# Kernel optimization log

Hardware: AMD Instinct MI355X
Metric: run time of the kernel (lower is better)

The kernel has to match this reference:

```python
import jax, jax.numpy as jnp
import numpy as np

N_NODES = 50000
N_EDGES = 500000
N_REL = 8
D = 128        # input_dim
A_DIM = 64     # attention_dim
D_OUT = 128    # output_dim


def setup_inputs() -> dict:
    key = jax.random.key(0)
    ks = jax.random.split(key, 10)
    h = jax.random.normal(ks[0], (N_NODES, D), jnp.float32)
    # relation gate tables: [R, 2*D, D]; first D rows act on dst (subject), last D on src (object)
    relations = jax.random.normal(ks[1], (N_REL, 2 * D, D), jnp.float32) * 0.05
    rel_attention = jax.random.normal(ks[2], (N_REL, A_DIM), jnp.float32) * 0.05
    W_a = jax.random.normal(ks[3], (A_DIM, 2 * D), jnp.float32) * 0.05
    b_a = jnp.zeros((A_DIM,), jnp.float32)
    W_lin = jax.random.normal(ks[4], (D_OUT, 2 * D), jnp.float32) * 0.05
    b_lin = jnp.zeros((D_OUT,), jnp.float32)
    src = jax.random.randint(ks[5], (N_EDGES,), 0, N_NODES, dtype=jnp.int32)
    dst = jax.random.randint(ks[6], (N_EDGES,), 0, N_NODES, dtype=jnp.int32)
    etype = jax.random.randint(ks[7], (N_EDGES,), 0, N_REL, dtype=jnp.int32)
    return {"h": h, "relations": relations, "rel_attention": rel_attention,
            "W_a": W_a, "b_a": b_a, "W_lin": W_lin, "b_lin": b_lin,
            "src": src, "dst": dst, "etype": etype}


def reference(h, relations, rel_attention, W_a, b_a, W_lin, b_lin, src, dst, etype):
    d = h.shape[-1]
    # --- gates: relation-indexed gather_mm (concat gate type) ---
    # Project every node through every relation once (R is small), then gather per edge.
    proj_dst = jnp.einsum('nd,rde->rne', h, relations[:, :d, :])   # [R, N, D] subject/dst side
    proj_src = jnp.einsum('nd,rde->rne', h, relations[:, d:, :])   # [R, N, D] object/src side
    gate = jax.nn.sigmoid(proj_dst[etype, dst] + proj_src[etype, src])  # [E, D]

    src_h = h[src]   # [E, D]
    dst_h = h[dst]   # [E, D]

    # --- gatv2 attention (predicates are zeroed in the module -> rel_attention[0]) ---
    a = jax.nn.leaky_relu(jnp.concatenate([dst_h, src_h], axis=-1) @ W_a.T + b_a)  # [E, A]
    score = (rel_attention[0] * a).sum(-1)  # [E]

    # --- edge_softmax over destination-node segments ---
    smax = jax.ops.segment_max(score, dst, num_segments=N_NODES)
    ex = jnp.exp(score - smax[dst])
    denom = jax.ops.segment_sum(ex, dst, num_segments=N_NODES)
    attn = ex / denom[dst]  # [E]

    # --- message = u_mul_e(h, attn*gate), reduce = sum over dst ---
    msg = src_h * (attn[:, None] * gate)                 # [E, D]
    h_N = jax.ops.segment_sum(msg, dst, num_segments=N_NODES)  # [N, D]

    # --- graphsage aggregate: LeakyReLU(W [h ; h_N] + b) ---
    out = jax.nn.leaky_relu(jnp.concatenate([h, h_N], axis=-1) @ W_lin.T + b_lin)
    return out
```

## Files before the change

kernel.cpp:

```cpp
#include <hip/hip_runtime.h>
#include <cstdint>
#include <cstddef>

constexpr int NNODES = 50000;
constexpr int NEDGES = 500000;
constexpr int NRELS  = 8;
constexpr int DIM    = 128;
constexpr int ADIM   = 64;
constexpr int TWOD   = 256;
constexpr int EPB    = 64;
constexpr float SLOPE = 0.01f;

constexpr int XPITCH = TWOD + 8;
constexpr int PPITCH = DIM + 8;
constexpr int MPITCH = DIM + 8;
constexpr int SPAD = NEDGES + 1024;

typedef __attribute__((ext_vector_type(8))) short short8;
typedef __attribute__((ext_vector_type(4))) float floatx4;

__device__ __forceinline__ unsigned short f2bf(float f) {
    unsigned u = __float_as_uint(f);
    unsigned r = u + 0x7FFFu + ((u >> 16) & 1u);
    return (unsigned short)(r >> 16);
}
__device__ __forceinline__ float bf2f(unsigned short b) {
    return __uint_as_float(((unsigned)b) << 16);
}

__global__ void k_init(int* __restrict__ srcS, int* __restrict__ histD,
                       int* __restrict__ cursorD, int* __restrict__ cnts) {
    int i = blockIdx.x * blockDim.x + threadIdx.x;
    int stride = gridDim.x * blockDim.x;
    for (int idx = i; idx < SPAD; idx += stride) srcS[idx] = -1;
    for (int idx = i; idx < NNODES; idx += stride) { histD[idx] = 0; cursorD[idx] = 0; }
    if (i < 16) cnts[i] = 0;
}

__global__ __launch_bounds__(256) void k_prep(const float* __restrict__ rel,
                                              const float* __restrict__ W_lin,
                                              const float* __restrict__ W_a,
                                              unsigned short* __restrict__ relT,
                                              unsigned short* __restrict__ Wl,
                                              unsigned short* __restrict__ Wa2) {
    __shared__ float ls[64][65];
    int b = blockIdx.x, t = threadIdx.x;
    if (b < 64) {
        int r = b >> 3, tile = b & 7;
        int d0 = (tile >> 1) * 64, o0 = (tile & 1) * 64;
        const float* rp = rel + ((size_t)r * TWOD + d0) * DIM + o0;
#pragma unroll
        for (int u = 0; u < 16; u++) {
            int v = u * 256 + t;
            int j = v & 63, i = v >> 6;
            ls[i][j] = rp[(size_t)i * DIM + j];
        }
        __syncthreads();
        unsigned short* wp = relT + ((size_t)r * DIM + o0) * TWOD + d0;
#pragma unroll
        for (int u = 0; u < 16; u++) {
            int v = u * 256 + t;
            int ii = v & 63, jj = v >> 6;
            wp[(size_t)jj * TWOD + ii] = f2bf(ls[ii][jj]);
        }
    } else {
        int idx = (b - 64) * 256 + t;
        if (idx < DIM * TWOD) {
            Wl[idx] = f2bf(W_lin[idx]);
        } else {
            int j = idx - DIM * TWOD;
            if (j < DIM * DIM) {
                int d = j & 127, o = j >> 7;
                float v = (o < ADIM) ? W_a[(size_t)o * TWOD + d]
                                     : W_a[(size_t)(o - ADIM) * TWOD + DIM + d];
                Wa2[j] = f2bf(v);
            }
        }
    }
}

__global__ void k_hist2(const int* __restrict__ ety, const int* __restrict__ dst,
                        int* __restrict__ cnt, int* __restrict__ histD) {
    __shared__ int hist[NRELS];
    int t = threadIdx.x;
    if (t < NRELS) hist[t] = 0;
    __syncthreads();
    int e = blockIdx.x * 256 + t;
    if (e < NEDGES) {
        atomicAdd(&hist[ety[e]], 1);
        atomicAdd(&histD[dst[e]], 1);
    }
    __syncthreads();
    if (t < NRELS && hist[t] > 0) atomicAdd(&cnt[t], hist[t]);
}

__global__ __launch_bounds__(1024) void k_scan(const int* __restrict__ histD,
                                               int* __restrict__ row_ptr,
                                               const int* __restrict__ cnt,
                                               int* __restrict__ offs) {
    __shared__ int ls[1024];
    const int t = threadIdx.x;
    const int CH = (NNODES + 1023) / 1024;
    const int base = t * CH;
    int s = 0;
    for (int j = 0; j < CH; j++) { int i = base + j; if (i < NNODES) s += histD[i]; }
    ls[t] = s;
    __syncthreads();
    for (int off = 1; off < 1024; off <<= 1) {
        int v = (t >= off) ? ls[t - off] : 0;
        __syncthreads();
        ls[t] += v;
        __syncthreads();
    }
    int run = (t == 0) ? 0 : ls[t - 1];
    for (int j = 0; j < CH; j++) {
        int i = base + j;
        if (i < NNODES) { row_ptr[i] = run; run += histD[i]; }
    }
    if (t == 1023) row_ptr[NNODES] = ls[1023];
    if (t == 0) {
        int off = 0;
        for (int r = 0; r < NRELS; r++) {
            offs[r] = off;
            off += ((cnt[r] + EPB - 1) / EPB) * EPB;
        }
    }
}

__global__ void k_dscatter(const int* __restrict__ ety, const int* __restrict__ src,
                           const int* __restrict__ dst, const int* __restrict__ row_ptr,
                           int* __restrict__ cursorD,
                           int* __restrict__ srcP, int* __restrict__ dstP,
                           int* __restrict__ etyP) {
    int e = blockIdx.x * 256 + threadIdx.x;
    if (e < NEDGES) {
        int dn = dst[e];
        int pos = row_ptr[dn] + atomicAdd(&cursorD[dn], 1);
        srcP[pos] = src[e];
        dstP[pos] = dn;
        etyP[pos] = ety[e];
    }
}

__global__ void k_scatter3(const int* __restrict__ srcP, const int* __restrict__ dstP,
                           const int* __restrict__ etyP, const int* __restrict__ offs,
                           int* __restrict__ cursorE,
                           int* __restrict__ srcS, int* __restrict__ dstS,
                           int* __restrict__ posS) {
    __shared__ int hist[NRELS];
    __shared__ int basew[NRELS];
    int t = threadIdx.x;
    if (t < NRELS) hist[t] = 0;
    __syncthreads();
    int p = blockIdx.x * 256 + t;
    int r = -1, rank = 0, sn = 0, dn = 0;
    if (p < NEDGES) {
        r = etyP[p]; sn = srcP[p]; dn = dstP[p];
        rank = atomicAdd(&hist[r], 1);
    }
    __syncthreads();
    if (t < NRELS && hist[t] > 0) basew[t] = atomicAdd(&cursorE[t], hist[t]);
    __syncthreads();
    if (p < NEDGES) {
        int s = offs[r] + basew[r] + rank;
        srcS[s] = sn;
        dstS[s] = dn;
        posS[s] = p;
    }
}

__global__ __launch_bounds__(256) void k_nodeproj(const float* __restrict__ h,
                                                  const unsigned short* __restrict__ Wa2,
                                                  unsigned short* __restrict__ proj16,
                                                  unsigned short* __restrict__ h16) {
    __shared__ unsigned short Xs[EPB * PPITCH];
    const int t = threadIdx.x;
    const int nb = blockIdx.x * 64;

#pragma unroll
    for (int u = 0; u < 4; u++) {
        int v = u * 256 + t;
        int i = v >> 4;
        int c = v & 15;
        int n = nb + i;
        bool ok = n < NNODES;
        if (!ok) n = NNODES - 1;
        const float4* hp = (const float4*)(h + (size_t)n * DIM + c * 8);
        float4 a = hp[0], b = hp[1];
        union { unsigned short us[8]; short8 s8; } pk;
        pk.us[0] = f2bf(a.x); pk.us[1] = f2bf(a.y); pk.us[2] = f2bf(a.z); pk.us[3] = f2bf(a.w);
        pk.us[4] = f2bf(b.x); pk.us[5] = f2bf(b.y); pk.us[6] = f2bf(b.z); pk.us[7] = f2bf(b.w);
        *(short8*)&Xs[i * PPITCH + c * 8] = pk.s8;
        if (ok) *(short8*)&h16[(size_t)n * DIM + c * 8] = pk.s8;
    }

    const int wave = t >> 6;
    const int lane = t & 63;
    const int q = lane >> 4;
    const int l16 = lane & 15;

    short8 Bf[2][4];
#pragma unroll
    for (int nn = 0; nn < 2; nn++) {
        int o = (wave * 2 + nn) * 16 + l16;
        const unsigned short* bp = Wa2 + (size_t)o * DIM + q * 8;
#pragma unroll
        for (int ks = 0; ks < 4; ks++) Bf[nn][ks] = *(const short8*)(bp + ks * 32);
    }

    __syncthreads();

    floatx4 acc[4][2];
#pragma unroll
    for (int m = 0; m < 4; m++)
#pragma unroll
        for (int nn = 0; nn < 2; nn++) acc[m][nn] = (floatx4)(0.0f);

#pragma unroll
    for (int ks = 0; ks < 4; ks++) {
        short8 Af[4];
        const unsigned short* xb = &Xs[l16 * PPITCH + ks * 32 + q * 8];
#pragma unroll
        for (int m = 0; m < 4; m++) Af[m] = *(const short8*)(xb + m * 16 * PPITCH);
#pragma unroll
        for (int m = 0; m < 4; m++)
#pragma unroll
            for (int nn = 0; nn < 2; nn++)
                acc[m][nn] = __builtin_amdgcn_mfma_f32_16x16x32_bf16(Af[m], Bf[nn][ks], acc[m][nn], 0, 0, 0);
    }

#pragma unroll
    for (int m = 0; m < 4; m++) {
        int ib = m * 16 + q * 4;
#pragma unroll
        for (int nn = 0; nn < 2; nn++) {
            int o = (wave * 2 + nn) * 16 + l16;
#pragma unroll
            for (int rg = 0; rg < 4; rg++) {
                int n = nb + ib + rg;
                if (n < NNODES) proj16[(size_t)n * DIM + o] = f2bf(acc[m][nn][rg]);
            }
        }
    }
}

__global__ __launch_bounds__(256) void k_score(const unsigned short* __restrict__ proj16,
                                               const float* __restrict__ b_a, const float* __restrict__ ratt,
                                               const int* __restrict__ srcP, const int* __restrict__ dstP,
                                               float* __restrict__ scoreP) {
    int p = blockIdx.x * 4 + (threadIdx.x >> 6);
    int lane = threadIdx.x & 63;
    if (p >= NEDGES) return;
    int sn = srcP[p], dn = dstP[p];
    float v = bf2f(proj16[(size_t)dn * DIM + lane]) + bf2f(proj16[(size_t)sn * DIM + ADIM + lane]) + b_a[lane];
    v = v > 0.0f ? v : SLOPE * v;
    v *= ratt[lane];
#pragma unroll
    for (int off = 32; off > 0; off >>= 1) v += __shfl_down(v, off);
    if (lane == 0) scoreP[p] = v;
}

__global__ __launch_bounds__(256) void k_segsoft(float* __restrict__ scoreP,
                                                 const int* __restrict__ row_ptr) {
    int n = blockIdx.x * 16 + (threadIdx.x >> 4);
    int l = threadIdx.x & 15;
    if (n >= NNODES) return;
    int p0 = row_ptr[n], p1 = row_ptr[n + 1];
    if (p0 >= p1) return;
    float m = -3.0e38f;
    for (int p = p0 + l; p < p1; p += 16) m = fmaxf(m, scoreP[p]);
#pragma unroll
    for (int off = 8; off > 0; off >>= 1) m = fmaxf(m, __shfl_xor(m, off, 16));
    float sum = 0.0f;
    for (int p = p0 + l; p < p1; p += 16) {
        float x = __expf(scoreP[p] - m);
        scoreP[p] = x;
        sum += x;
    }
#pragma unroll
    for (int off = 8; off > 0; off >>= 1) sum += __shfl_xor(sum, off, 16);
    float inv = 1.0f / sum;
    for (int p = p0 + l; p < p1; p += 16) scoreP[p] *= inv;
}

__global__ __launch_bounds__(256) void k_gate_msg(
    const unsigned short* __restrict__ h16, const unsigned short* __restrict__ relT,
    const int* __restrict__ srcS, const int* __restrict__ dstS, const int* __restrict__ posS,
    const int* __restrict__ offs,
    unsigned short* __restrict__ msgbuf) {
    __shared__ unsigned short Xs[EPB * XPITCH];
    __shared__ unsigned short Ms[EPB * MPITCH];
    __shared__ int srcn_s[EPB];
    __shared__ int dstn_s[EPB];
    __shared__ int pos_s[EPB];
    __shared__ int val_s[EPB];

    const int t = threadIdx.x;
    const int base = blockIdx.x * EPB;

    if (t < EPB) {
        int s = base + t;
        int sv = srcS[s];
        int valid = sv >= 0;
        val_s[t] = valid;
        srcn_s[t] = valid ? sv : 0;
        dstn_s[t] = valid ? dstS[s] : 0;
        pos_s[t] = valid ? posS[s] : 0;
    }
    __syncthreads();
    if (!val_s[0]) return;

    int r = 0;
#pragma unroll
    for (int i = 1; i < NRELS; i++) if (base >= offs[i]) r = i;

#pragma unroll
    for (int u = 0; u < 8; u++) {
        int v = u * 256 + t;
        int i = v >> 5;
        int c = v & 31;
        int node = (c < 16) ? dstn_s[i] : srcn_s[i];
        *(short8*)&Xs[i * XPITCH + c * 8] = *(const short8*)&h16[(size_t)node * DIM + (c & 15) * 8];
    }

    const int wave = t >> 6;
    const int lane = t & 63;
    const int q = lane >> 4;
    const int l16 = lane & 15;

    short8 Bf[2][8];
#pragma unroll
    for (int nn = 0; nn < 2; nn++) {
        int o = (wave * 2 + nn) * 16 + l16;
        const unsigned short* bp = relT + ((size_t)r * DIM + o) * TWOD + q * 8;
#pragma unroll
        for (int ks = 0; ks < 8; ks++) Bf[nn][ks] = *(const short8*)(bp + ks * 32);
    }

    __syncthreads();

    floatx4 acc[4][2];
#pragma unroll
    for (int m = 0; m < 4; m++)
#pragma unroll
        for (int nn = 0; nn < 2; nn++) acc[m][nn] = (floatx4)(0.0f);

#pragma unroll
    for (int ks = 0; ks < 8; ks++) {
        short8 Af[4];
        const unsigned short* xb = &Xs[l16 * XPITCH + ks * 32 + q * 8];
#pragma unroll
        for (int m = 0; m < 4; m++) Af[m] = *(const short8*)(xb + m * 16 * XPITCH);
#pragma unroll
        for (int m = 0; m < 4; m++)
#pragma unroll
            for (int nn = 0; nn < 2; nn++)
                acc[m][nn] = __builtin_amdgcn_mfma_f32_16x16x32_bf16(Af[m], Bf[nn][ks], acc[m][nn], 0, 0, 0);
    }

#pragma unroll
    for (int m = 0; m < 4; m++) {
        int ib = m * 16 + q * 4;
#pragma unroll
        for (int nn = 0; nn < 2; nn++) {
            int o = (wave * 2 + nn) * 16 + l16;
#pragma unroll
            for (int rg = 0; rg < 4; rg++) {
                int i = ib + rg;
                float g = 1.0f / (1.0f + __expf(-acc[m][nn][rg]));
                float sh = bf2f(Xs[i * XPITCH + DIM + o]);
                Ms[i * MPITCH + o] = f2bf(sh * g);
            }
        }
    }
    __syncthreads();
#pragma unroll
    for (int u = 0; u < 4; u++) {
        int v = u * 256 + t;
        int i = v >> 4;
        int c = v & 15;
        if (!val_s[i]) continue;
        short8 val = *(const short8*)&Ms[i * MPITCH + c * 8];
        *(short8*)&msgbuf[(size_t)pos_s[i] * DIM + c * 8] = val;
    }
}

__global__ __launch_bounds__(256) void k_aggr(const unsigned short* __restrict__ msgbuf,
                                              const float* __restrict__ attP,
                                              const int* __restrict__ row_ptr,
                                              unsigned short* __restrict__ hN16) {
    int n = blockIdx.x * 4 + (threadIdx.x >> 6);
    int lane = threadIdx.x & 63;
    if (n >= NNODES) return;
    int p0 = row_ptr[n], p1 = row_ptr[n + 1];
    float a0 = 0.0f, a1 = 0.0f;
    for (int p = p0; p < p1; p++) {
        float at = attP[p];
        unsigned v = *(const unsigned*)&msgbuf[(size_t)p * DIM + lane * 2];
        a0 += at * bf2f((unsigned short)(v & 0xFFFFu));
        a1 += at * bf2f((unsigned short)(v >> 16));
    }
    unsigned o = (unsigned)f2bf(a0) | ((unsigned)f2bf(a1) << 16);
    *(unsigned*)&hN16[(size_t)n * DIM + lane * 2] = o;
}

__global__ __launch_bounds__(256) void k_out(const unsigned short* __restrict__ h16,
                                             const unsigned short* __restrict__ hN16,
                                             const unsigned short* __restrict__ Wl,
                                             const float* __restrict__ b_lin,
                                             float* __restrict__ out) {
    __shared__ unsigned short Xs[EPB * XPITCH];
    const int t = threadIdx.x;
    const int nb = blockIdx.x * 64;

#pragma unroll
    for (int u = 0; u < 8; u++) {
        int v = u * 256 + t;
        int i = v >> 5;
        int c = v & 31;
        int n = nb + i;
        if (n >= NNODES) n = NNODES - 1;
        const unsigned short* srcp = (c < 16) ? h16 : hN16;
        *(short8*)&Xs[i * XPITCH + c * 8] = *(const short8*)&srcp[(size_t)n * DIM + (c & 15) * 8];
    }

    const int wave = t >> 6;
    const int lane = t & 63;
    const int q = lane >> 4;
    const int l16 = lane & 15;

    short8 Bf[2][8];
#pragma unroll
    for (int nn = 0; nn < 2; nn++) {
        int o = (wave * 2 + nn) * 16 + l16;
        const unsigned short* bp = Wl + (size_t)o * TWOD + q * 8;
#pragma unroll
        for (int ks = 0; ks < 8; ks++) Bf[nn][ks] = *(const short8*)(bp + ks * 32);
    }

    __syncthreads();

    floatx4 acc[4][2];
#pragma unroll
    for (int m = 0; m < 4; m++)
#pragma unroll
        for (int nn = 0; nn < 2; nn++) acc[m][nn] = (floatx4)(0.0f);

#pragma unroll
    for (int ks = 0; ks < 8; ks++) {
        short8 Af[4];
        const unsigned short* xb = &Xs[l16 * XPITCH + ks * 32 + q * 8];
#pragma unroll
        for (int m = 0; m < 4; m++) Af[m] = *(const short8*)(xb + m * 16 * XPITCH);
#pragma unroll
        for (int m = 0; m < 4; m++)
#pragma unroll
            for (int nn = 0; nn < 2; nn++)
                acc[m][nn] = __builtin_amdgcn_mfma_f32_16x16x32_bf16(Af[m], Bf[nn][ks], acc[m][nn], 0, 0, 0);
    }

#pragma unroll
    for (int m = 0; m < 4; m++) {
        int ib = m * 16 + q * 4;
#pragma unroll
        for (int nn = 0; nn < 2; nn++) {
            int o = (wave * 2 + nn) * 16 + l16;
            float bl = b_lin[o];
#pragma unroll
            for (int rg = 0; rg < 4; rg++) {
                int n = nb + ib + rg;
                if (n < NNODES) {
                    float val = acc[m][nn][rg] + bl;
                    val = val > 0.0f ? val : SLOPE * val;
                    out[(size_t)n * DIM + o] = val;
                }
            }
        }
    }
}

extern "C" void kernel_launch(void* const* d_in, const int* in_sizes, int n_in,
                              void* d_out, int out_size, void* d_ws, size_t ws_size,
                              hipStream_t stream) {
    const float* h     = (const float*)d_in[0];
    const float* rel   = (const float*)d_in[1];
    const float* ratt  = (const float*)d_in[2];
    const float* W_a   = (const float*)d_in[3];
    const float* b_a   = (const float*)d_in[4];
    const float* W_lin = (const float*)d_in[5];
    const float* b_lin = (const float*)d_in[6];
    const int* src = (const int*)d_in[7];
    const int* dst = (const int*)d_in[8];
    const int* ety = (const int*)d_in[9];
    float* out = (float*)d_out;

    float* scoreP = (float*)d_ws;
    unsigned short* h16    = (unsigned short*)(scoreP + NEDGES);
    unsigned short* proj16 = h16 + (size_t)NNODES * DIM;
    unsigned short* hN16   = proj16 + (size_t)NNODES * DIM;
    unsigned short* relT   = hN16 + (size_t)NNODES * DIM;
    unsigned short* Wl     = relT + (size_t)NRELS * DIM * TWOD;
    unsigned short* Wa2    = Wl + (size_t)DIM * TWOD;
    int* srcS    = (int*)(Wa2 + (size_t)DIM * DIM);
    int* dstS    = srcS + SPAD;
    int* posS    = dstS + SPAD;
    int* srcP    = posS + SPAD;
    int* dstP    = srcP + NEDGES;
    int* etyP    = dstP + NEDGES;
    int* row_ptr = etyP + NEDGES;
    int* histD   = row_ptr + (NNODES + 1);
    int* cursorD = histD + NNODES;
    int* cnts    = cursorD + NNODES;
    int* offs    = cnts + 16;
    unsigned short* msgbuf = (unsigned short*)(((uintptr_t)(offs + 8) + 255) & ~(uintptr_t)255);

    k_init<<<2048, 256, 0, stream>>>(srcS, histD, cursorD, cnts);
    k_prep<<<64 + (DIM * TWOD + DIM * DIM + 255) / 256, 256, 0, stream>>>(
        rel, W_lin, W_a, relT, Wl, Wa2);
    k_hist2<<<(NEDGES + 255) / 256, 256, 0, stream>>>(ety, dst, cnts, histD);
    k_scan<<<1, 1024, 0, stream>>>(histD, row_ptr, cnts, offs);
    k_dscatter<<<(NEDGES + 255) / 256, 256, 0, stream>>>(
        ety, src, dst, row_ptr, cursorD, srcP, dstP, etyP);
    k_nodeproj<<<(NNODES + 63) / 64, 256, 0, stream>>>(h, Wa2, proj16, h16);
    k_scatter3<<<(NEDGES + 255) / 256, 256, 0, stream>>>(
        srcP, dstP, etyP, offs, cnts + 8, srcS, dstS, posS);
    k_score<<<(NEDGES + 3) / 4, 256, 0, stream>>>(proj16, b_a, ratt, srcP, dstP, scoreP);
    k_segsoft<<<(NNODES + 15) / 16, 256, 0, stream>>>(scoreP, row_ptr);
    k_gate_msg<<<(NEDGES + 8 * EPB + EPB - 1) / EPB, 256, 0, stream>>>(
        h16, relT, srcS, dstS, posS, offs, msgbuf);
    k_aggr<<<(NNODES + 3) / 4, 256, 0, stream>>>(msgbuf, scoreP, row_ptr, hN16);
    k_out<<<(NNODES + 63) / 64, 256, 0, stream>>>(h16, hN16, Wl, b_lin, out);
}
```

Before: 553.8 us.

## Fuse attention score into gate-message kernel and pack edge metadata into int4

Attention scores are now computed per edge inside the gate/message kernel. An extra MFMA pass multiplies the already-gathered [dst;src] bf16 tile by W_a, which replaces the per-node projection kernel and the separate score kernel. Edge metadata (src, dst, type, position) is packed into int4 records so each scatter stage does one vector access instead of several scalar arrays, and the message is written back into the staging tile in place of a second shared buffer. In exchange, the attention GEMM is redone per edge rather than per node (about ten times more FLOPs), and the gate kernel carries extra register and shared-memory pressure.

```diff
diff --git a/kernel.cpp b/kernel.cpp
--- a/kernel.cpp
+++ b/kernel.cpp
@@ -12,8 +12,6 @@
 constexpr float SLOPE = 0.01f;
 
 constexpr int XPITCH = TWOD + 8;
-constexpr int PPITCH = DIM + 8;
-constexpr int MPITCH = DIM + 8;
 constexpr int SPAD = NEDGES + 1024;
 
 typedef __attribute__((ext_vector_type(8))) short short8;
@@ -28,11 +26,11 @@
     return __uint_as_float(((unsigned)b) << 16);
 }
 
-__global__ void k_init(int* __restrict__ srcS, int* __restrict__ histD,
+__global__ void k_init(int4* __restrict__ sMeta, int* __restrict__ histD,
                        int* __restrict__ cursorD, int* __restrict__ cnts) {
     int i = blockIdx.x * blockDim.x + threadIdx.x;
     int stride = gridDim.x * blockDim.x;
-    for (int idx = i; idx < SPAD; idx += stride) srcS[idx] = -1;
+    for (int idx = i; idx < SPAD; idx += stride) sMeta[idx] = make_int4(-1, 0, 0, 0);
     for (int idx = i; idx < NNODES; idx += stride) { histD[idx] = 0; cursorD[idx] = 0; }
     if (i < 16) cnts[i] = 0;
 }
@@ -42,7 +40,7 @@
                                               const float* __restrict__ W_a,
                                               unsigned short* __restrict__ relT,
                                               unsigned short* __restrict__ Wl,
-                                              unsigned short* __restrict__ Wa2) {
+                                              unsigned short* __restrict__ Wa16) {
     __shared__ float ls[64][65];
     int b = blockIdx.x, t = threadIdx.x;
     if (b < 64) {
@@ -69,13 +67,20 @@
             Wl[idx] = f2bf(W_lin[idx]);
         } else {
             int j = idx - DIM * TWOD;
-            if (j < DIM * DIM) {
-                int d = j & 127, o = j >> 7;
-                float v = (o < ADIM) ? W_a[(size_t)o * TWOD + d]
-                                     : W_a[(size_t)(o - ADIM) * TWOD + DIM + d];
-                Wa2[j] = f2bf(v);
-            }
-        }
+            if (j < ADIM * TWOD) Wa16[j] = f2bf(W_a[j]);
+        }
+    }
+}
+
+__global__ void k_h16(const float* __restrict__ h, unsigned short* __restrict__ h16) {
+    int i = blockIdx.x * 256 + threadIdx.x;
+    if (i < NNODES * DIM / 8) {
+        const float4* hp = (const float4*)(h + (size_t)i * 8);
+        float4 a = hp[0], b = hp[1];
+        union { unsigned short us[8]; short8 s8; } pk;
+        pk.us[0] = f2bf(a.x); pk.us[1] = f2bf(a.y); pk.us[2] = f2bf(a.z); pk.us[3] = f2bf(a.w);
+        pk.us[4] = f2bf(b.x); pk.us[5] = f2bf(b.y); pk.us[6] = f2bf(b.z); pk.us[7] = f2bf(b.w);
+        *(short8*)&h16[(size_t)i * 8] = pk.s8;
     }
 }
 
@@ -129,33 +134,28 @@
 
 __global__ void k_dscatter(const int* __restrict__ ety, const int* __restrict__ src,
                            const int* __restrict__ dst, const int* __restrict__ row_ptr,
-                           int* __restrict__ cursorD,
-                           int* __restrict__ srcP, int* __restrict__ dstP,
-                           int* __restrict__ etyP) {
+                           int* __restrict__ cursorD, int4* __restrict__ meta4) {
     int e = blockIdx.x * 256 + threadIdx.x;
     if (e < NEDGES) {
         int dn = dst[e];
         int pos = row_ptr[dn] + atomicAdd(&cursorD[dn], 1);
-        srcP[pos] = src[e];
-        dstP[pos] = dn;
-        etyP[pos] = ety[e];
-    }
-}
-
-__global__ void k_scatter3(const int* __restrict__ srcP, const int* __restrict__ dstP,
-                           const int* __restrict__ etyP, const int* __restrict__ offs,
-                           int* __restrict__ cursorE,
-                           int* __restrict__ srcS, int* __restrict__ dstS,
-                           int* __restrict__ posS) {
+        meta4[pos] = make_int4(src[e], dn, ety[e], 0);
+    }
+}
+
+__global__ void k_scatter3(const int4* __restrict__ meta4, const int* __restrict__ offs,
+                           int* __restrict__ cursorE, int4* __restrict__ sMeta) {
     __shared__ int hist[NRELS];
     __shared__ int basew[NRELS];
     int t = threadIdx.x;
     if (t < NRELS) hist[t] = 0;
     __syncthreads();
     int p = blockIdx.x * 256 + t;
-    int r = -1, rank = 0, sn = 0, dn = 0;
+    int r = -1, rank = 0;
+    int4 m4 = make_int4(0, 0, 0, 0);
     if (p < NEDGES) {
-        r = etyP[p]; sn = srcP[p]; dn = dstP[p];
+        m4 = meta4[p];
+        r = m4.z;
         rank = atomicAdd(&hist[r], 1);
     }
     __syncthreads();
@@ -163,101 +163,152 @@
     __syncthreads();
     if (p < NEDGES) {
         int s = offs[r] + basew[r] + rank;
-        srcS[s] = sn;
-        dstS[s] = dn;
-        posS[s] = p;
-    }
-}
-
-__global__ __launch_bounds__(256) void k_nodeproj(const float* __restrict__ h,
-                                                  const unsigned short* __restrict__ Wa2,
-                                                  unsigned short* __restrict__ proj16,
-                                                  unsigned short* __restrict__ h16) {
-    __shared__ unsigned short Xs[EPB * PPITCH];
+        sMeta[s] = make_int4(m4.x, m4.y, p, 0);
+    }
+}
+
+__global__ __launch_bounds__(256) void k_gate_msg(
+    const unsigned short* __restrict__ h16, const unsigned short* __restrict__ relT,
+    const unsigned short* __restrict__ Wa16,
+    const int4* __restrict__ sMeta, const float* __restrict__ b_a,
+    const float* __restrict__ ratt, const int* __restrict__ offs,
+    unsigned short* __restrict__ msgbuf, float* __restrict__ scoreP) {
+    __shared__ unsigned short Xs[EPB * XPITCH];
+    __shared__ int srcn_s[EPB];
+    __shared__ int dstn_s[EPB];
+    __shared__ int pos_s[EPB];
+    __shared__ int val_s[EPB];
+    __shared__ float scoreW[EPB][4];
+
     const int t = threadIdx.x;
-    const int nb = blockIdx.x * 64;
+    const int base = blockIdx.x * EPB;
+
+    if (t < EPB) {
+        int4 m4 = sMeta[base + t];
+        int valid = m4.x >= 0;
+        val_s[t] = valid;
+        srcn_s[t] = valid ? m4.x : 0;
+        dstn_s[t] = valid ? m4.y : 0;
+        pos_s[t] = valid ? m4.z : 0;
+    }
+    __syncthreads();
+    if (!val_s[0]) return;
+
+    int r = 0;
+#pragma unroll
+    for (int i = 1; i < NRELS; i++) if (base >= offs[i]) r = i;
+
+#pragma unroll
+    for (int u = 0; u < 8; u++) {
+        int v = u * 256 + t;
+        int i = v >> 5;
+        int c = v & 31;
+        int node = (c < 16) ? dstn_s[i] : srcn_s[i];
+        *(short8*)&Xs[i * XPITCH + c * 8] = *(const short8*)&h16[(size_t)node * DIM + (c & 15) * 8];
+    }
+
+    const int wave = t >> 6;
+    const int lane = t & 63;
+    const int q = lane >> 4;
+    const int l16 = lane & 15;
+
+    short8 Bf[2][8];
+#pragma unroll
+    for (int nn = 0; nn < 2; nn++) {
+        int o = (wave * 2 + nn) * 16 + l16;
+        const unsigned short* bp = relT + ((size_t)r * DIM + o) * TWOD + q * 8;
+#pragma unroll
+        for (int ks = 0; ks < 8; ks++) Bf[nn][ks] = *(const short8*)(bp + ks * 32);
+    }
+
+    __syncthreads();
+
+    floatx4 acc[4][2];
+#pragma unroll
+    for (int m = 0; m < 4; m++)
+#pragma unroll
+        for (int nn = 0; nn < 2; nn++) acc[m][nn] = (floatx4)(0.0f);
+
+#pragma unroll
+    for (int ks = 0; ks < 8; ks++) {
+        short8 Af[4];
+        const unsigned short* xb = &Xs[l16 * XPITCH + ks * 32 + q * 8];
+#pragma unroll
+        for (int m = 0; m < 4; m++) Af[m] = *(const short8*)(xb + m * 16 * XPITCH);
+#pragma unroll
+        for (int m = 0; m < 4; m++)
+#pragma unroll
+            for (int nn = 0; nn < 2; nn++)
+                acc[m][nn] = __builtin_amdgcn_mfma_f32_16x16x32_bf16(Af[m], Bf[nn][ks], acc[m][nn], 0, 0, 0);
+    }
+
+    const int o16 = wave * 16 + l16;
+    floatx4 accS[4];
+#pragma unroll
+    for (int m = 0; m < 4; m++) accS[m] = (floatx4)(0.0f);
+    {
+        const unsigned short* wb = Wa16 + (size_t)o16 * TWOD + q * 8;
+#pragma unroll
+        for (int ks = 0; ks < 8; ks++) {
+            short8 BS = *(const short8*)(wb + ks * 32);
+            short8 Af[4];
+            const unsigned short* xb = &Xs[l16 * XPITCH + ks * 32 + q * 8];
+#pragma unroll
+            for (int m = 0; m < 4; m++) Af[m] = *(const short8*)(xb + m * 16 * XPITCH);
+#pragma unroll
+            for (int m = 0; m < 4; m++)
+                accS[m] = __builtin_amdgcn_mfma_f32_16x16x32_bf16(Af[m], BS, accS[m], 0, 0, 0);
+        }
+    }
+
+    __syncthreads();
+
+    {
+        float ba = b_a[o16];
+        float ra = ratt[o16];
+#pragma unroll
+        for (int m = 0; m < 4; m++) {
+#pragma unroll
+            for (int rg = 0; rg < 4; rg++) {
+                float v = accS[m][rg] + ba;
+                v = v > 0.0f ? v : SLOPE * v;
+                v *= ra;
+#pragma unroll
+                for (int off = 8; off > 0; off >>= 1) v += __shfl_xor(v, off, 16);
+                if (l16 == 0) scoreW[m * 16 + q * 4 + rg][wave] = v;
+            }
+        }
+    }
+
+#pragma unroll
+    for (int m = 0; m < 4; m++) {
+        int ib = m * 16 + q * 4;
+#pragma unroll
+        for (int nn = 0; nn < 2; nn++) {
+            int o = (wave * 2 + nn) * 16 + l16;
+#pragma unroll
+            for (int rg = 0; rg < 4; rg++) {
+                int i = ib + rg;
+                float g = 1.0f / (1.0f + __expf(-acc[m][nn][rg]));
+                float sh = bf2f(Xs[i * XPITCH + DIM + o]);
+                Xs[i * XPITCH + o] = f2bf(sh * g);
+            }
+        }
+    }
+    __syncthreads();
 
 #pragma unroll
     for (int u = 0; u < 4; u++) {
         int v = u * 256 + t;
         int i = v >> 4;
         int c = v & 15;
-        int n = nb + i;
-        bool ok = n < NNODES;
-        if (!ok) n = NNODES - 1;
-        const float4* hp = (const float4*)(h + (size_t)n * DIM + c * 8);
-        float4 a = hp[0], b = hp[1];
-        union { unsigned short us[8]; short8 s8; } pk;
-        pk.us[0] = f2bf(a.x); pk.us[1] = f2bf(a.y); pk.us[2] = f2bf(a.z); pk.us[3] = f2bf(a.w);
-        pk.us[4] = f2bf(b.x); pk.us[5] = f2bf(b.y); pk.us[6] = f2bf(b.z); pk.us[7] = f2bf(b.w);
-        *(short8*)&Xs[i * PPITCH + c * 8] = pk.s8;
-        if (ok) *(short8*)&h16[(size_t)n * DIM + c * 8] = pk.s8;
-    }
-
-    const int wave = t >> 6;
-    const int lane = t & 63;
-    const int q = lane >> 4;
-    const int l16 = lane & 15;
-
-    short8 Bf[2][4];
-#pragma unroll
-    for (int nn = 0; nn < 2; nn++) {
-        int o = (wave * 2 + nn) * 16 + l16;
-        const unsigned short* bp = Wa2 + (size_t)o * DIM + q * 8;
-#pragma unroll
-        for (int ks = 0; ks < 4; ks++) Bf[nn][ks] = *(const short8*)(bp + ks * 32);
-    }
-
-    __syncthreads();
-
-    floatx4 acc[4][2];
-#pragma unroll
-    for (int m = 0; m < 4; m++)
-#pragma unroll
-        for (int nn = 0; nn < 2; nn++) acc[m][nn] = (floatx4)(0.0f);
-
-#pragma unroll
-    for (int ks = 0; ks < 4; ks++) {
-        short8 Af[4];
-        const unsigned short* xb = &Xs[l16 * PPITCH + ks * 32 + q * 8];
-#pragma unroll
-        for (int m = 0; m < 4; m++) Af[m] = *(const short8*)(xb + m * 16 * PPITCH);
-#pragma unroll
-        for (int m = 0; m < 4; m++)
-#pragma unroll
-            for (int nn = 0; nn < 2; nn++)
-                acc[m][nn] = __builtin_amdgcn_mfma_f32_16x16x32_bf16(Af[m], Bf[nn][ks], acc[m][nn], 0, 0, 0);
-    }
-
-#pragma unroll
-    for (int m = 0; m < 4; m++) {
-        int ib = m * 16 + q * 4;
-#pragma unroll
-        for (int nn = 0; nn < 2; nn++) {
-            int o = (wave * 2 + nn) * 16 + l16;
-#pragma unroll
-            for (int rg = 0; rg < 4; rg++) {
-                int n = nb + ib + rg;
-                if (n < NNODES) proj16[(size_t)n * DIM + o] = f2bf(acc[m][nn][rg]);
-            }
-        }
-    }
-}
-
-__global__ __launch_bounds__(256) void k_score(const unsigned short* __restrict__ proj16,
-                                               const float* __restrict__ b_a, const float* __restrict__ ratt,
-                                               const int* __restrict__ srcP, const int* __restrict__ dstP,
-                                               float* __restrict__ scoreP) {
-    int p = blockIdx.x * 4 + (threadIdx.x >> 6);
-    int lane = threadIdx.x & 63;
-    if (p >= NEDGES) return;
-    int sn = srcP[p], dn = dstP[p];
-    float v = bf2f(proj16[(size_t)dn * DIM + lane]) + bf2f(proj16[(size_t)sn * DIM + ADIM + lane]) + b_a[lane];
-    v = v > 0.0f ? v : SLOPE * v;
-    v *= ratt[lane];
-#pragma unroll
-    for (int off = 32; off > 0; off >>= 1) v += __shfl_down(v, off);
-    if (lane == 0) scoreP[p] = v;
+        if (!val_s[i]) continue;
+        short8 val = *(const short8*)&Xs[i * XPITCH + c * 8];
+        *(short8*)&msgbuf[(size_t)pos_s[i] * DIM + c * 8] = val;
+    }
+    if (t < EPB && val_s[t]) {
+        scoreP[pos_s[t]] = scoreW[t][0] + scoreW[t][1] + scoreW[t][2] + scoreW[t][3];
+    }
 }
 
 __global__ __launch_bounds__(256) void k_segsoft(float* __restrict__ scoreP,
@@ -281,108 +332,6 @@
     for (int off = 8; off > 0; off >>= 1) sum += __shfl_xor(sum, off, 16);
     float inv = 1.0f / sum;
     for (int p = p0 + l; p < p1; p += 16) scoreP[p] *= inv;
-}
-
-__global__ __launch_bounds__(256) void k_gate_msg(
-    const unsigned short* __restrict__ h16, const unsigned short* __restrict__ relT,
-    const int* __restrict__ srcS, const int* __restrict__ dstS, const int* __restrict__ posS,
-    const int* __restrict__ offs,
-    unsigned short* __restrict__ msgbuf) {
-    __shared__ unsigned short Xs[EPB * XPITCH];
-    __shared__ unsigned short Ms[EPB * MPITCH];
-    __shared__ int srcn_s[EPB];
-    __shared__ int dstn_s[EPB];
-    __shared__ int pos_s[EPB];
-    __shared__ int val_s[EPB];
-
-    const int t = threadIdx.x;
-    const int base = blockIdx.x * EPB;
-
-    if (t < EPB) {
-        int s = base + t;
-        int sv = srcS[s];
-        int valid = sv >= 0;
-        val_s[t] = valid;
-        srcn_s[t] = valid ? sv : 0;
-        dstn_s[t] = valid ? dstS[s] : 0;
-        pos_s[t] = valid ? posS[s] : 0;
-    }
-    __syncthreads();
-    if (!val_s[0]) return;
-
-    int r = 0;
-#pragma unroll
-    for (int i = 1; i < NRELS; i++) if (base >= offs[i]) r = i;
-
-#pragma unroll
-    for (int u = 0; u < 8; u++) {
-        int v = u * 256 + t;
-        int i = v >> 5;
-        int c = v & 31;
-        int node = (c < 16) ? dstn_s[i] : srcn_s[i];
-        *(short8*)&Xs[i * XPITCH + c * 8] = *(const short8*)&h16[(size_t)node * DIM + (c & 15) * 8];
-    }
-
-    const int wave = t >> 6;
-    const int lane = t & 63;
-    const int q = lane >> 4;
-    const int l16 = lane & 15;
-
-    short8 Bf[2][8];
-#pragma unroll
-    for (int nn = 0; nn < 2; nn++) {
-        int o = (wave * 2 + nn) * 16 + l16;
-        const unsigned short* bp = relT + ((size_t)r * DIM + o) * TWOD + q * 8;
-#pragma unroll
-        for (int ks = 0; ks < 8; ks++) Bf[nn][ks] = *(const short8*)(bp + ks * 32);
-    }
-
-    __syncthreads();
-
-    floatx4 acc[4][2];
-#pragma unroll
-    for (int m = 0; m < 4; m++)
-#pragma unroll
-        for (int nn = 0; nn < 2; nn++) acc[m][nn] = (floatx4)(0.0f);
-
-#pragma unroll
-    for (int ks = 0; ks < 8; ks++) {
-        short8 Af[4];
-        const unsigned short* xb = &Xs[l16 * XPITCH + ks * 32 + q * 8];
-#pragma unroll
-        for (int m = 0; m < 4; m++) Af[m] = *(const short8*)(xb + m * 16 * XPITCH);
-#pragma unroll
-        for (int m = 0; m < 4; m++)
-#pragma unroll
-            for (int nn = 0; nn < 2; nn++)
-                acc[m][nn] = __builtin_amdgcn_mfma_f32_16x16x32_bf16(Af[m], Bf[nn][ks], acc[m][nn], 0, 0, 0);
-    }
-
-#pragma unroll
-    for (int m = 0; m < 4; m++) {
-        int ib = m * 16 + q * 4;
-#pragma unroll
-        for (int nn = 0; nn < 2; nn++) {
-            int o = (wave * 2 + nn) * 16 + l16;
-#pragma unroll
-            for (int rg = 0; rg < 4; rg++) {
-                int i = ib + rg;
-                float g = 1.0f / (1.0f + __expf(-acc[m][nn][rg]));
-                float sh = bf2f(Xs[i * XPITCH + DIM + o]);
-                Ms[i * MPITCH + o] = f2bf(sh * g);
-            }
-        }
-    }
-    __syncthreads();
-#pragma unroll
-    for (int u = 0; u < 4; u++) {
-        int v = u * 256 + t;
-        int i = v >> 4;
-        int c = v & 15;
-        if (!val_s[i]) continue;
-        short8 val = *(const short8*)&Ms[i * MPITCH + c * 8];
-        *(short8*)&msgbuf[(size_t)pos_s[i] * DIM + c * 8] = val;
-    }
 }
 
 __global__ __launch_bounds__(256) void k_aggr(const unsigned short* __restrict__ msgbuf,
@@ -495,39 +444,32 @@
     float* out = (float*)d_out;
 
     float* scoreP = (float*)d_ws;
-    unsigned short* h16    = (unsigned short*)(scoreP + NEDGES);
-    unsigned short* proj16 = h16 + (size_t)NNODES * DIM;
-    unsigned short* hN16   = proj16 + (size_t)NNODES * DIM;
-    unsigned short* relT   = hN16 + (size_t)NNODES * DIM;
-    unsigned short* Wl     = relT + (size_t)NRELS * DIM * TWOD;
-    unsigned short* Wa2    = Wl + (size_t)DIM * TWOD;
-    int* srcS    = (int*)(Wa2 + (size_t)DIM * DIM);
-    int* dstS    = srcS + SPAD;
-    int* posS    = dstS + SPAD;
-    int* srcP    = posS + SPAD;
-    int* dstP    = srcP + NEDGES;
-    int* etyP    = dstP + NEDGES;
-    int* row_ptr = etyP + NEDGES;
+    unsigned short* h16  = (unsigned short*)(scoreP + NEDGES);
+    unsigned short* hN16 = h16 + (size_t)NNODES * DIM;
+    unsigned short* relT = hN16 + (size_t)NNODES * DIM;
+    unsigned short* Wl   = relT + (size_t)NRELS * DIM * TWOD;
+    unsigned short* Wa16 = Wl + (size_t)DIM * TWOD;
+    int4* meta4  = (int4*)(Wa16 + (size_t)ADIM * TWOD);
+    int4* sMeta  = meta4 + NEDGES;
+    int* row_ptr = (int*)(sMeta + SPAD);
     int* histD   = row_ptr + (NNODES + 1);
     int* cursorD = histD + NNODES;
     int* cnts    = cursorD + NNODES;
     int* offs    = cnts + 16;
     unsigned short* msgbuf = (unsigned short*)(((uintptr_t)(offs + 8) + 255) & ~(uintptr_t)255);
 
-    k_init<<<2048, 256, 0, stream>>>(srcS, histD, cursorD, cnts);
-    k_prep<<<64 + (DIM * TWOD + DIM * DIM + 255) / 256, 256, 0, stream>>>(
-        rel, W_lin, W_a, relT, Wl, Wa2);
+    k_init<<<2048, 256, 0, stream>>>(sMeta, histD, cursorD, cnts);
+    k_prep<<<64 + (DIM * TWOD + ADIM * TWOD + 255) / 256, 256, 0, stream>>>(
+        rel, W_lin, W_a, relT, Wl, Wa16);
+    k_h16<<<(NNODES * DIM / 8 + 255) / 256, 256, 0, stream>>>(h, h16);
     k_hist2<<<(NEDGES + 255) / 256, 256, 0, stream>>>(ety, dst, cnts, histD);
     k_scan<<<1, 1024, 0, stream>>>(histD, row_ptr, cnts, offs);
     k_dscatter<<<(NEDGES + 255) / 256, 256, 0, stream>>>(
-        ety, src, dst, row_ptr, cursorD, srcP, dstP, etyP);
-    k_nodeproj<<<(NNODES + 63) / 64, 256, 0, stream>>>(h, Wa2, proj16, h16);
-    k_scatter3<<<(NEDGES + 255) / 256, 256, 0, stream>>>(
-        srcP, dstP, etyP, offs, cnts + 8, srcS, dstS, posS);
-    k_score<<<(NEDGES + 3) / 4, 256, 0, stream>>>(proj16, b_a, ratt, srcP, dstP, scoreP);
+        ety, src, dst, row_ptr, cursorD, meta4);
+    k_scatter3<<<(NEDGES + 255) / 256, 256, 0, stream>>>(meta4, offs, cnts + 8, sMeta);
+    k_gate_msg<<<(NEDGES + 8 * EPB + EPB - 1) / EPB, 256, 0, stream>>>(
+        h16, relT, Wa16, sMeta, b_a, ratt, offs, msgbuf, scoreP);
     k_segsoft<<<(NNODES + 15) / 16, 256, 0, stream>>>(scoreP, row_ptr);
-    k_gate_msg<<<(NEDGES + 8 * EPB + EPB - 1) / EPB, 256, 0, stream>>>(
-        h16, relT, srcS, dstS, posS, offs, msgbuf);
     k_aggr<<<(NNODES + 3) / 4, 256, 0, stream>>>(msgbuf, scoreP, row_ptr, hN16);
     k_out<<<(NNODES + 63) / 64, 256, 0, stream>>>(h16, hN16, Wl, b_lin, out);
 }
```

New measurement: 547.4 us. No clear change (-1.1%).
